# Performance work log

Measured on AMD Instinct MI355X. Metric: run time of the kernel, lower is better.

## Reference

```python
import jax, jax.numpy as jnp
import numpy as np

B, S, HID = 4, 2048, 2048
NH, NKV, HD = 16, 4, 128
GROUPS = NH // NKV
THETA = 10000.0
SCALING = 1.0
SCALE = HD ** -0.5


def setup_inputs() -> dict:
    key = jax.random.key(0)
    k1, k2, k3 = jax.random.split(key, 3)
    hidden_states = jax.random.normal(k1, (B, S, HID), dtype=jnp.float32)
    # stored as [in, out] so x @ W matches torch Linear(x) with W = weight.T
    W_qkv = jax.random.normal(k2, (HID, (NH + 2 * NKV) * HD), dtype=jnp.float32) * (HID ** -0.5)
    W_o = jax.random.normal(k3, (HID, HID), dtype=jnp.float32) * (HID ** -0.5)
    return {"hidden_states": hidden_states, "W_qkv": W_qkv, "W_o": W_o}


def _rope_tables(seq_len, dtype):
    inv_freq = 1.0 / (THETA ** (jnp.arange(0, HD, 2, dtype=jnp.float32) / HD))
    t = jnp.arange(seq_len, dtype=jnp.float32) / SCALING
    freqs = jnp.einsum("s,d->sd", t, inv_freq)          # [S, HD/2]
    emb = jnp.concatenate([freqs, freqs], axis=-1)        # [S, HD]
    return jnp.cos(emb).astype(dtype), jnp.sin(emb).astype(dtype)


def _rotate_half(x):
    x1, x2 = jnp.split(x, 2, axis=-1)
    return jnp.concatenate([-x2, x1], axis=-1)


def _apply_rope(x, cos, sin):
    # x: [B, H, S, D]; cos/sin: [S, D]
    return x * cos[None, None] + _rotate_half(x) * sin[None, None]


def reference(hidden_states, W_qkv, W_o):
    b, s, _ = hidden_states.shape
    qkv = hidden_states @ W_qkv                           # [B, S, (NH+2NKV)*HD]
    q, k, v = jnp.split(qkv, [NH * HD, (NH + NKV) * HD], axis=-1)
    q = q.reshape(b, s, NH, HD).transpose(0, 2, 1, 3)      # [B, NH, S, D]
    k = k.reshape(b, s, NKV, HD).transpose(0, 2, 1, 3)     # [B, NKV, S, D]
    v = v.reshape(b, s, NKV, HD).transpose(0, 2, 1, 3)

    cos, sin = _rope_tables(s, hidden_states.dtype)
    q = _apply_rope(q, cos, sin)
    k = _apply_rope(k, cos, sin)

    # GQA attention without materializing expanded K/V
    qg = q.reshape(b, NKV, GROUPS, s, HD)                  # [B, NKV, G, Sq, D]
    scores = jnp.einsum("bkgqd,bkKd->bkgqK", qg, k) * SCALE
    causal = jnp.tril(jnp.ones((s, s), dtype=bool))
    scores = jnp.where(causal[None, None, None], scores, jnp.finfo(scores.dtype).min)
    probs = jax.nn.softmax(scores, axis=-1)
    out = jnp.einsum("bkgqK,bkKd->bkgqd", probs, v)        # [B, NKV, G, Sq, D]
    out = out.reshape(b, NH, s, HD).transpose(0, 2, 1, 3).reshape(b, s, HID)
    return out @ W_o
```

## Files before the change

kernel.cpp:

```cpp
#include <hip/hip_runtime.h>

#define B_ 4
#define S_ 2048
#define HID_ 2048
#define NH_ 16
#define NKV_ 4
#define HD_ 128
#define NTOK (B_ * S_)
#define QKV_N 3072
#define KO_N 512
#define SCALE_ 0.08838834764831845f
#define QSC_ 0.12751743f
#define LOG2_10K 13.287712379549449f
#define NEG_ -30000.0f

typedef __attribute__((ext_vector_type(8))) short short8;
typedef __attribute__((ext_vector_type(4))) short short4v;
typedef __attribute__((ext_vector_type(4))) float f32x4;
typedef unsigned short ushort_t;
typedef unsigned int uint32;

__device__ __forceinline__ float sanit(float x) {
    if (!(x == x)) x = 0.0f;
    return fminf(fmaxf(x, -65504.0f), 65504.0f);
}
__device__ __forceinline__ ushort_t f2bf(float f) {
    union { float f; uint32 u; } c; c.f = f;
    uint32 u = c.u;
    u += 0x7fffu + ((u >> 16) & 1u);
    return (ushort_t)(u >> 16);
}
__device__ __forceinline__ ushort_t f2bf_s(float f) { return f2bf(sanit(f)); }
__device__ __forceinline__ float bf2f(ushort_t h) {
    union { float f; uint32 u; } c; c.u = ((uint32)h) << 16;
    return c.f;
}

__device__ __forceinline__ void gl16(const ushort_t* g, ushort_t* l) {
    __builtin_amdgcn_global_load_lds(
        (__attribute__((address_space(1))) void*)g,
        (__attribute__((address_space(3))) void*)l, 16, 0, 0);
}

__global__ void convx_kernel(const float* __restrict__ X, ushort_t* __restrict__ Xb) {
    size_t i = (size_t)blockIdx.x * blockDim.x + threadIdx.x;
    const float4 a = *(const float4*)(X + i * 8);
    const float4 b = *(const float4*)(X + i * 8 + 4);
    short8 p;
    p[0] = (short)f2bf(a.x); p[1] = (short)f2bf(a.y);
    p[2] = (short)f2bf(a.z); p[3] = (short)f2bf(a.w);
    p[4] = (short)f2bf(b.x); p[5] = (short)f2bf(b.y);
    p[6] = (short)f2bf(b.z); p[7] = (short)f2bf(b.w);
    *(short8*)(Xb + i * 8) = p;
}

__global__ void wtrans_kernel(const float* __restrict__ W, ushort_t* __restrict__ Wt,
                              int K, int N) {
    __shared__ float tile[32][33];
    const int n0 = blockIdx.x * 32;
    const int k0 = blockIdx.y * 32;
    const int t  = threadIdx.x;
    const int r  = t >> 3;
    const int c  = (t & 7) * 4;
    const float4 v = *(const float4*)(W + (size_t)(k0 + r) * N + n0 + c);
    tile[r][c] = v.x; tile[r][c + 1] = v.y; tile[r][c + 2] = v.z; tile[r][c + 3] = v.w;
    __syncthreads();
    short4v p;
    p[0] = (short)f2bf(tile[c][r]);
    p[1] = (short)f2bf(tile[c + 1][r]);
    p[2] = (short)f2bf(tile[c + 2][r]);
    p[3] = (short)f2bf(tile[c + 3][r]);
    *(short4v*)(Wt + (size_t)(n0 + r) * K + k0 + c) = p;
}

__global__ void ropetab_kernel(float* __restrict__ ct, float* __restrict__ st) {
    int p = blockIdx.x * blockDim.x + threadIdx.x;
    int s = p >> 6, d = p & 63;
    float inv = exp2f(-(float)d * (LOG2_10K / 64.0f));
    float ang = (float)s * inv;
    float sn, cs;
    sincosf(ang, &sn, &cs);
    ct[p] = cs; st[p] = sn;
}

template <int SPLIT>
__global__ __launch_bounds__(256, 2) void gemm_bt(
    const ushort_t* __restrict__ A, const ushort_t* __restrict__ Bt,
    void* __restrict__ C0, ushort_t* __restrict__ C1, ushort_t* __restrict__ C2,
    int M, int N, int K) {
    __shared__ __align__(16) ushort_t As[128 * 64];
    __shared__ __align__(16) ushort_t Bs[128 * 64];

    const int tid  = threadIdx.x;
    const int lane = tid & 63;
    const int w    = tid >> 6;
    const int wm   = (w >> 1) * 64;
    const int wn   = (w & 1) * 64;
    const int m0   = blockIdx.y * 128;
    const int n0   = blockIdx.x * 128;
    const int col  = lane & 15;
    const int quad = lane >> 4;

    f32x4 acc[4][4] = {};

    const ushort_t* agp[4];
    const ushort_t* bgp[4];
    ushort_t* lap[4];
    ushort_t* lbp[4];
#pragma unroll
    for (int i = 0; i < 4; ++i) {
        int c  = i * 256 + tid;
        int rw = c >> 3;
        int kc = (c & 7) * 8;
        agp[i] = A  + (size_t)(m0 + rw) * K + kc;
        bgp[i] = Bt + (size_t)(n0 + rw) * K + kc;
        lap[i] = &As[c * 8];
        lbp[i] = &Bs[c * 8];
    }

    for (int k0 = 0; k0 < K; k0 += 64) {
        __syncthreads();
#pragma unroll
        for (int i = 0; i < 4; ++i) gl16(agp[i] + k0, lap[i]);
#pragma unroll
        for (int i = 0; i < 4; ++i) gl16(bgp[i] + k0, lbp[i]);
        __syncthreads();

#pragma unroll
        for (int kk = 0; kk < 2; ++kk) {
            short8 af[4], bfr[4];
#pragma unroll
            for (int mt = 0; mt < 4; ++mt)
                af[mt] = *(const short8*)&As[(wm + mt * 16 + col) * 64 + kk * 32 + quad * 8];
#pragma unroll
            for (int nt = 0; nt < 4; ++nt)
                bfr[nt] = *(const short8*)&Bs[(wn + nt * 16 + col) * 64 + kk * 32 + quad * 8];
#pragma unroll
            for (int mt = 0; mt < 4; ++mt)
#pragma unroll
                for (int nt = 0; nt < 4; ++nt)
                    acc[mt][nt] = __builtin_amdgcn_mfma_f32_16x16x32_bf16(
                        af[mt], bfr[nt], acc[mt][nt], 0, 0, 0);
        }
    }

    if (SPLIT) {
        if (n0 >= 2560) {
#pragma unroll
            for (int mt = 0; mt < 4; ++mt)
#pragma unroll
                for (int nt = 0; nt < 4; ++nt) {
                    int cc   = n0 + wn + nt * 16 + col - 2560;
                    int row0 = m0 + wm + mt * 16 + quad * 4;
                    short4v p;
#pragma unroll
                    for (int r = 0; r < 4; ++r) p[r] = (short)f2bf_s(acc[mt][nt][r]);
                    *(short4v*)&C2[(size_t)cc * NTOK + row0] = p;
                }
        } else {
            ushort_t* dst;
            int ldc, coff;
            if (n0 >= 2048) { dst = C1; ldc = KO_N; coff = 2048; }
            else            { dst = (ushort_t*)C0; ldc = HID_; coff = 0; }
#pragma unroll
            for (int mt = 0; mt < 4; ++mt)
#pragma unroll
                for (int nt = 0; nt < 4; ++nt)
#pragma unroll
                    for (int r = 0; r < 4; ++r) {
                        int row = m0 + wm + mt * 16 + quad * 4 + r;
                        int cc  = n0 + wn + nt * 16 + col - coff;
                        dst[(size_t)row * ldc + cc] = f2bf_s(acc[mt][nt][r]);
                    }
        }
    } else {
        float* dst = (float*)C0;
#pragma unroll
        for (int mt = 0; mt < 4; ++mt)
#pragma unroll
            for (int nt = 0; nt < 4; ++nt)
#pragma unroll
                for (int r = 0; r < 4; ++r) {
                    int row = m0 + wm + mt * 16 + quad * 4 + r;
                    int cc  = n0 + wn + nt * 16 + col;
                    dst[(size_t)row * N + cc] = sanit(acc[mt][nt][r]);
                }
    }
}

__global__ void rope_kernel(ushort_t* __restrict__ qbuf, ushort_t* __restrict__ kb,
                            const float* __restrict__ ct, const float* __restrict__ st) {
    int p = blockIdx.x * blockDim.x + threadIdx.x;
    int d0   = (p & 7) * 8;
    int rest = p >> 3;
    int head = rest % 20;
    int tok  = rest / 20;
    int s    = tok & (S_ - 1);

    ushort_t* base;
    float sc;
    if (head < 16) { base = qbuf + (size_t)tok * HID_ + head * HD_ + d0; sc = QSC_; }
    else           { base = kb   + (size_t)tok * KO_N + (head - 16) * HD_ + d0; sc = 1.0f; }

    short8 x1v = *(const short8*)base;
    short8 x2v = *(const short8*)(base + 64);
    const float* cp = ct + s * 64 + d0;
    const float* sp = st + s * 64 + d0;
    short8 r1, r2;
#pragma unroll
    for (int e = 0; e < 8; ++e) {
        float x1 = bf2f((ushort_t)x1v[e]);
        float x2 = bf2f((ushort_t)x2v[e]);
        float cs = cp[e], sn = sp[e];
        r1[e] = (short)f2bf_s((x1 * cs - x2 * sn) * sc);
        r2[e] = (short)f2bf_s((x2 * cs + x1 * sn) * sc);
    }
    *(short8*)base        = r1;
    *(short8*)(base + 64) = r2;
}

__global__ __launch_bounds__(512, 4) void flash_kernel(
    const ushort_t* __restrict__ qbuf, const ushort_t* __restrict__ kb,
    const ushort_t* __restrict__ vtg, ushort_t* __restrict__ obuf) {
    __shared__ __align__(16) ushort_t Ks[64][136];
    __shared__ __align__(16) ushort_t Vt[128][72];
    __shared__ __align__(16) ushort_t Ps[8][16][72];

    const int tid  = threadIdx.x;
    const int lane = tid & 63;
    const int w    = tid >> 6;
    const int col  = lane & 15;
    const int quad = lane >> 4;
    const int q0   = (S_ / 128 - 1 - blockIdx.x) * 128;
    const int h    = blockIdx.y;
    const int b    = blockIdx.z;
    const int kvh  = h >> 2;
    const int bS   = b * S_;

    const int wr    = q0 + w * 16;
    const int wmax  = wr + 15;
    const int i_row = wr + quad * 4;

    short8 qf[4];
    {
        const ushort_t* qp = qbuf + (size_t)(bS + wr + col) * HID_
                             + h * HD_ + quad * 8;
#pragma unroll
        for (int kt = 0; kt < 4; ++kt) qf[kt] = *(const short8*)(qp + kt * 32);
    }

    short8 vone;
#pragma unroll
    for (int e = 0; e < 8; ++e) vone[e] = (short)0x3F80;

    float m_i[4];
#pragma unroll
    for (int r = 0; r < 4; ++r) m_i[r] = NEG_;
    f32x4 o[8] = {};
    f32x4 lsum = {};

    const int ntiles = q0 / 64 + 2;

    const int jr = tid >> 3;
    const int kd = (tid & 7) * 16;
    const int vd = tid >> 2;
    const int vj = (tid & 3) * 16;

    const ushort_t* kgb = kb + (size_t)(bS + jr) * KO_N + kvh * HD_ + kd;
    const ushort_t* vgb = vtg + (size_t)(kvh * HD_ + vd) * NTOK + bS + vj;

    float4 pk0, pk1, pv0, pv1;
    pk0 = *(const float4*)(kgb);
    pk1 = *(const float4*)(kgb + 8);
    pv0 = *(const float4*)(vgb);
    pv1 = *(const float4*)(vgb + 8);
    *(float4*)&Ks[jr][kd]     = pk0;
    *(float4*)&Ks[jr][kd + 8] = pk1;
    *(float4*)&Vt[vd][vj]     = pv0;
    *(float4*)&Vt[vd][vj + 8] = pv1;
    __syncthreads();

    for (int t = 0; t < ntiles; ++t) {
        const int j0 = t * 64;
        const bool pre = (t + 1 < ntiles);
        if (pre) {
            const ushort_t* kgn = kgb + (size_t)(j0 + 64) * KO_N;
            const ushort_t* vgn = vgb + (j0 + 64);
            pk0 = *(const float4*)(kgn);
            pk1 = *(const float4*)(kgn + 8);
            pv0 = *(const float4*)(vgn);
            pv1 = *(const float4*)(vgn + 8);
        }

        if (j0 <= wmax) {
            f32x4 s[4] = {};
#pragma unroll
            for (int ct = 0; ct < 4; ++ct)
#pragma unroll
                for (int kt = 0; kt < 4; ++kt) {
                    short8 kf = *(const short8*)&Ks[ct * 16 + col][kt * 32 + quad * 8];
                    s[ct] = __builtin_amdgcn_mfma_f32_16x16x32_bf16(qf[kt], kf, s[ct], 0, 0, 0);
                }

            if (j0 + 64 > wr) {
#pragma unroll
                for (int ct = 0; ct < 4; ++ct) {
                    int jg = j0 + ct * 16 + col;
#pragma unroll
                    for (int r = 0; r < 4; ++r)
                        if (jg > i_row + r) s[ct][r] = NEG_;
                }
            }

            float mx[4];
#pragma unroll
            for (int r = 0; r < 4; ++r) {
                float m = fmaxf(fmaxf(s[0][r], s[1][r]), fmaxf(s[2][r], s[3][r]));
#pragma unroll
                for (int off = 1; off < 16; off <<= 1)
                    m = fmaxf(m, __shfl_xor(m, off, 64));
                mx[r] = m;
            }
            int ok = 1;
#pragma unroll
            for (int r = 0; r < 4; ++r) ok &= (mx[r] <= m_i[r] + 8.0f) ? 1 : 0;
            if (!__all(ok)) {
#pragma unroll
                for (int r = 0; r < 4; ++r) {
                    float mn = fmaxf(m_i[r], mx[r]);
                    float a  = exp2f(m_i[r] - mn);
                    m_i[r] = mn;
                    lsum[r] *= a;
#pragma unroll
                    for (int dt = 0; dt < 8; ++dt) o[dt][r] *= a;
                }
            }
#pragma unroll
            for (int ct = 0; ct < 4; ++ct)
#pragma unroll
                for (int r = 0; r < 4; ++r)
                    Ps[w][quad * 4 + r][ct * 16 + col] = f2bf(exp2f(s[ct][r] - m_i[r]));

#pragma unroll
            for (int kt = 0; kt < 2; ++kt) {
                short8 pf = *(const short8*)&Ps[w][col][kt * 32 + quad * 8];
#pragma unroll
                for (int dt = 0; dt < 8; ++dt) {
                    short8 vf = *(const short8*)&Vt[dt * 16 + col][kt * 32 + quad * 8];
                    o[dt] = __builtin_amdgcn_mfma_f32_16x16x32_bf16(pf, vf, o[dt], 0, 0, 0);
                }
                lsum = __builtin_amdgcn_mfma_f32_16x16x32_bf16(pf, vone, lsum, 0, 0, 0);
            }
        }

        __syncthreads();
        if (pre) {
            *(float4*)&Ks[jr][kd]     = pk0;
            *(float4*)&Ks[jr][kd + 8] = pk1;
            *(float4*)&Vt[vd][vj]     = pv0;
            *(float4*)&Vt[vd][vj + 8] = pv1;
            __syncthreads();
        }
    }

#pragma unroll
    for (int r = 0; r < 4; ++r) {
        float inv = 1.0f / fmaxf(lsum[r], 1e-30f);
        ushort_t* op = obuf + (size_t)(bS + i_row + r) * HID_ + h * HD_;
#pragma unroll
        for (int dt = 0; dt < 8; ++dt)
            op[dt * 16 + col] = f2bf_s(o[dt][r] * inv);
    }
}

extern "C" void kernel_launch(void* const* d_in, const int* in_sizes, int n_in,
                              void* d_out, int out_size, void* d_ws, size_t ws_size,
                              hipStream_t stream) {
    const float* X    = (const float*)d_in[0];
    const float* Wqkv = (const float*)d_in[1];
    const float* Wo   = (const float*)d_in[2];

    ushort_t* qb  = (ushort_t*)d_out;
    ushort_t* xh  = (ushort_t*)d_out + (size_t)NTOK * HID_;
    ushort_t* kb  = (ushort_t*)d_ws;
    ushort_t* vtg = kb + (size_t)NTOK * KO_N;
    ushort_t* wqt = vtg + (size_t)NTOK * KO_N;
    ushort_t* wot = (ushort_t*)d_ws + (size_t)NTOK * HID_;
    float*    ctab = (float*)(wot + (size_t)HID_ * HID_);
    float*    stab = ctab + (size_t)S_ * 64;
    ushort_t* oa  = (ushort_t*)d_ws;

    convx_kernel<<<NTOK * HID_ / (256 * 8), 256, 0, stream>>>(X, xh);
    wtrans_kernel<<<dim3(QKV_N / 32, HID_ / 32), 256, 0, stream>>>(Wqkv, wqt, HID_, QKV_N);
    wtrans_kernel<<<dim3(HID_ / 32, HID_ / 32), 256, 0, stream>>>(Wo, wot, HID_, HID_);
    ropetab_kernel<<<(S_ * 64) / 256, 256, 0, stream>>>(ctab, stab);
    gemm_bt<1><<<dim3(QKV_N / 128, NTOK / 128), 256, 0, stream>>>(
        xh, wqt, qb, kb, vtg, NTOK, QKV_N, HID_);
    rope_kernel<<<(NTOK * 20 * 8) / 256, 256, 0, stream>>>(qb, kb, ctab, stab);
    flash_kernel<<<dim3(S_ / 128, NH_, B_), 512, 0, stream>>>(qb, kb, vtg, xh);
    hipMemcpyAsync(oa, xh, (size_t)NTOK * HID_ * sizeof(ushort_t),
                   hipMemcpyDeviceToDevice, stream);
    gemm_bt<0><<<dim3(HID_ / 128, NTOK / 128), 256, 0, stream>>>(
        oa, wot, d_out, nullptr, nullptr, NTOK, HID_, HID_);
}
```

Measured before the change: 624.9 us.

## Enlarge GEMM tile to 256 rows, use DPP row max, skip attention-output copy

```diff
diff --git a/kernel.cpp b/kernel.cpp
--- a/kernel.cpp
+++ b/kernel.cpp
@@ -40,6 +40,20 @@
     __builtin_amdgcn_global_load_lds(
         (__attribute__((address_space(1))) void*)g,
         (__attribute__((address_space(3))) void*)l, 16, 0, 0);
+}
+
+__device__ __forceinline__ float dpp_max16(float x) {
+    union { float f; int i; } c, t;
+    c.f = x;
+    t.i = __builtin_amdgcn_update_dpp(0, c.i, 0xB1, 0xf, 0xf, true);
+    c.f = fmaxf(c.f, t.f);
+    t.i = __builtin_amdgcn_update_dpp(0, c.i, 0x4E, 0xf, 0xf, true);
+    c.f = fmaxf(c.f, t.f);
+    t.i = __builtin_amdgcn_update_dpp(0, c.i, 0x141, 0xf, 0xf, true);
+    c.f = fmaxf(c.f, t.f);
+    t.i = __builtin_amdgcn_update_dpp(0, c.i, 0x140, 0xf, 0xf, true);
+    c.f = fmaxf(c.f, t.f);
+    return c.f;
 }
 
 __global__ void convx_kernel(const float* __restrict__ X, ushort_t* __restrict__ Xb) {
@@ -84,11 +98,11 @@
 }
 
 template <int SPLIT>
-__global__ __launch_bounds__(256, 2) void gemm_bt(
+__global__ __launch_bounds__(512, 2) void gemm_bt(
     const ushort_t* __restrict__ A, const ushort_t* __restrict__ Bt,
     void* __restrict__ C0, ushort_t* __restrict__ C1, ushort_t* __restrict__ C2,
     int M, int N, int K) {
-    __shared__ __align__(16) ushort_t As[128 * 64];
+    __shared__ __align__(16) ushort_t As[256 * 64];
     __shared__ __align__(16) ushort_t Bs[128 * 64];
 
     const int tid  = threadIdx.x;
@@ -96,7 +110,7 @@
     const int w    = tid >> 6;
     const int wm   = (w >> 1) * 64;
     const int wn   = (w & 1) * 64;
-    const int m0   = blockIdx.y * 128;
+    const int m0   = blockIdx.y * 256;
     const int n0   = blockIdx.x * 128;
     const int col  = lane & 15;
     const int quad = lane >> 4;
@@ -104,17 +118,23 @@
     f32x4 acc[4][4] = {};
 
     const ushort_t* agp[4];
-    const ushort_t* bgp[4];
+    const ushort_t* bgp[2];
     ushort_t* lap[4];
-    ushort_t* lbp[4];
+    ushort_t* lbp[2];
 #pragma unroll
     for (int i = 0; i < 4; ++i) {
-        int c  = i * 256 + tid;
+        int c  = i * 512 + tid;
         int rw = c >> 3;
         int kc = (c & 7) * 8;
-        agp[i] = A  + (size_t)(m0 + rw) * K + kc;
+        agp[i] = A + (size_t)(m0 + rw) * K + kc;
+        lap[i] = &As[c * 8];
+    }
+#pragma unroll
+    for (int i = 0; i < 2; ++i) {
+        int c  = i * 512 + tid;
+        int rw = c >> 3;
+        int kc = (c & 7) * 8;
         bgp[i] = Bt + (size_t)(n0 + rw) * K + kc;
-        lap[i] = &As[c * 8];
         lbp[i] = &Bs[c * 8];
     }
 
@@ -123,7 +143,7 @@
 #pragma unroll
         for (int i = 0; i < 4; ++i) gl16(agp[i] + k0, lap[i]);
 #pragma unroll
-        for (int i = 0; i < 4; ++i) gl16(bgp[i] + k0, lbp[i]);
+        for (int i = 0; i < 2; ++i) gl16(bgp[i] + k0, lbp[i]);
         __syncthreads();
 
 #pragma unroll
@@ -314,13 +334,9 @@
 
             float mx[4];
 #pragma unroll
-            for (int r = 0; r < 4; ++r) {
-                float m = fmaxf(fmaxf(s[0][r], s[1][r]), fmaxf(s[2][r], s[3][r]));
-#pragma unroll
-                for (int off = 1; off < 16; off <<= 1)
-                    m = fmaxf(m, __shfl_xor(m, off, 64));
-                mx[r] = m;
-            }
+            for (int r = 0; r < 4; ++r)
+                mx[r] = dpp_max16(fmaxf(fmaxf(s[0][r], s[1][r]),
+                                        fmaxf(s[2][r], s[3][r])));
             int ok = 1;
 #pragma unroll
             for (int r = 0; r < 4; ++r) ok &= (mx[r] <= m_i[r] + 8.0f) ? 1 : 0;
@@ -388,18 +404,25 @@
     ushort_t* wot = (ushort_t*)d_ws + (size_t)NTOK * HID_;
     float*    ctab = (float*)(wot + (size_t)HID_ * HID_);
     float*    stab = ctab + (size_t)S_ * 64;
-    ushort_t* oa  = (ushort_t*)d_ws;
+    ushort_t* ohi  = (ushort_t*)(stab + (size_t)S_ * 64);
+
+    const size_t osize  = (size_t)NTOK * HID_ * sizeof(ushort_t);
+    const size_t need   = (size_t)((char*)ohi - (char*)d_ws) + osize;
+    const bool   direct = (ws_size >= need);
+
+    ushort_t* oflash = direct ? ohi : xh;
+    ushort_t* oa     = direct ? ohi : (ushort_t*)d_ws;
 
     convx_kernel<<<NTOK * HID_ / (256 * 8), 256, 0, stream>>>(X, xh);
     wtrans_kernel<<<dim3(QKV_N / 32, HID_ / 32), 256, 0, stream>>>(Wqkv, wqt, HID_, QKV_N);
     wtrans_kernel<<<dim3(HID_ / 32, HID_ / 32), 256, 0, stream>>>(Wo, wot, HID_, HID_);
     ropetab_kernel<<<(S_ * 64) / 256, 256, 0, stream>>>(ctab, stab);
-    gemm_bt<1><<<dim3(QKV_N / 128, NTOK / 128), 256, 0, stream>>>(
+    gemm_bt<1><<<dim3(QKV_N / 128, NTOK / 256), 512, 0, stream>>>(
         xh, wqt, qb, kb, vtg, NTOK, QKV_N, HID_);
     rope_kernel<<<(NTOK * 20 * 8) / 256, 256, 0, stream>>>(qb, kb, ctab, stab);
-    flash_kernel<<<dim3(S_ / 128, NH_, B_), 512, 0, stream>>>(qb, kb, vtg, xh);
-    hipMemcpyAsync(oa, xh, (size_t)NTOK * HID_ * sizeof(ushort_t),
-                   hipMemcpyDeviceToDevice, stream);
-    gemm_bt<0><<<dim3(HID_ / 128, NTOK / 128), 256, 0, stream>>>(
+    flash_kernel<<<dim3(S_ / 128, NH_, B_), 512, 0, stream>>>(qb, kb, vtg, oflash);
+    if (!direct)
+        hipMemcpyAsync(oa, oflash, osize, hipMemcpyDeviceToDevice, stream);
+    gemm_bt<0><<<dim3(HID_ / 128, NTOK / 256), 512, 0, stream>>>(
         oa, wot, d_out, nullptr, nullptr, NTOK, HID_, HID_);
 }
```

Measured after the change: 582.8 us. 1.07x faster.
